# Kernel tuning notes

Measured on AMD Instinct MI355X. Metric: run time of the kernel, lower is better.

Reference implementation:

```python
import jax, jax.numpy as jnp
import numpy as np
from jax import lax

B, L, E = 2, 2048, 1024          # batch, seq_len, embed_dim
NL = 2                            # n_layers
DI = 2 * E                        # d_inner (expand=2)
DS = 16                           # d_state
DC = 4                            # d_conv
DTR = (E + 15) // 16              # dt_rank = ceil(d_model/16) = 64


def setup_inputs() -> dict:
    key = jax.random.key(0)
    ks = jax.random.split(key, 12)
    s = 0.02
    inp = {
        "x": jax.random.normal(ks[0], (B, L, E), jnp.float32),
        "pos_embed": jax.random.normal(ks[1], (L, E), jnp.float32) * s,
        "in_proj_w": jax.random.normal(ks[2], (NL, 2 * DI, E), jnp.float32) * s,
        "conv_w": jax.random.normal(ks[3], (NL, DI, DC), jnp.float32) * s,
        "conv_b": jnp.zeros((NL, DI), jnp.float32),
        "x_proj_w": jax.random.normal(ks[4], (NL, DTR + 2 * DS, DI), jnp.float32) * s,
        "dt_proj_w": jax.random.normal(ks[5], (NL, DI, DTR), jnp.float32) * s,
        "dt_bias": jax.random.normal(ks[6], (NL, DI), jnp.float32) * 0.1,
        "A_log": jnp.broadcast_to(jnp.log(jnp.arange(1, DS + 1, dtype=jnp.float32)), (NL, DI, DS)) + 0.0,
        "D_skip": jnp.ones((NL, DI), jnp.float32),
        "out_proj_w": jax.random.normal(ks[7], (NL, E, DI), jnp.float32) * s,
        "norm_w": jnp.ones((NL, E), jnp.float32),
    }
    return inp


def _rmsnorm(x, w, eps=1e-6):
    return x * lax.rsqrt(jnp.mean(x * x, axis=-1, keepdims=True) + eps) * w


def _mamba(h, in_w, cw, cb, xw, dtw, dtb, A_log, Dp, ow):
    # h: (B, L, E)
    xz = jnp.einsum("ble,de->bld", h, in_w)          # (B, L, 2*DI)
    xc, z = jnp.split(xz, 2, axis=-1)                 # each (B, L, DI)
    # causal depthwise conv1d (kernel DC)
    xp = jnp.pad(xc, ((0, 0), (DC - 1, 0), (0, 0)))
    xconv = cb
    acc = jnp.zeros_like(xc)
    for k in range(DC):
        acc = acc + cw[:, k] * xp[:, k:k + xc.shape[1], :]
    xc = jax.nn.silu(acc + cb)
    # input-dependent SSM params
    x_dbl = jnp.einsum("bld,rd->blr", xc, xw)         # (B, L, DTR+2*DS)
    dt, Bm, C = jnp.split(x_dbl, [DTR, DTR + DS], axis=-1)
    delta = jax.nn.softplus(jnp.einsum("blr,dr->bld", dt, dtw) + dtb)  # (B, L, DI)
    A = -jnp.exp(A_log)                               # (DI, DS)

    def step(hst, inp):
        d, bm, c, u = inp                             # (B,DI),(B,DS),(B,DS),(B,DI)
        hst = jnp.exp(d[..., None] * A) * hst + (d * u)[..., None] * bm[:, None, :]
        y = jnp.einsum("bdn,bn->bd", hst, c)
        return hst, y

    h0 = jnp.zeros((h.shape[0], DI, DS), h.dtype)
    _, ys = lax.scan(step, h0, (delta.swapaxes(0, 1), Bm.swapaxes(0, 1),
                                C.swapaxes(0, 1), xc.swapaxes(0, 1)))
    y = ys.swapaxes(0, 1) + xc * Dp                   # (B, L, DI)
    y = y * jax.nn.silu(z)
    return jnp.einsum("bld,ed->ble", y, ow)


def reference(x, pos_embed, in_proj_w, conv_w, conv_b, x_proj_w, dt_proj_w,
              dt_bias, A_log, D_skip, out_proj_w, norm_w):
    h = x + pos_embed[None, :x.shape[1]]
    for i in range(in_proj_w.shape[0]):
        y = _mamba(h, in_proj_w[i], conv_w[i], conv_b[i], x_proj_w[i],
                   dt_proj_w[i], dt_bias[i], A_log[i], D_skip[i], out_proj_w[i])
        h = _rmsnorm(y + h, norm_w[i])
    return h
```

## Files before the change

### kernel.cpp

```cpp
#include <hip/hip_runtime.h>

#define B_   2
#define L_   2048
#define E_   1024
#define NL_  2
#define DI_  2048
#define DS_  16
#define DC_  4
#define DTR_ 64
#define NXD_ 96
#define M_   (B_ * L_)
#define NCH_ 64
#define LC_  32

typedef __attribute__((ext_vector_type(8))) short bf16x8;
typedef __attribute__((ext_vector_type(4))) float f32x4;

__device__ __forceinline__ float bf2f(unsigned short u) {
    return __uint_as_float(((unsigned)u) << 16);
}
__device__ __forceinline__ unsigned short f2bf(float f) {
    unsigned u = __float_as_uint(f);
    u += 0x7fff + ((u >> 16) & 1);
    return (unsigned short)(u >> 16);
}

#define LOG2E_ 1.44269504f
#define LN2_   0.69314718f

__device__ __forceinline__ float sigmoidf_(float x) {
    return __builtin_amdgcn_rcpf(1.f + __builtin_amdgcn_exp2f(-x * LOG2E_));
}
__device__ __forceinline__ float softplusf_(float x) {
    float e = __builtin_amdgcn_exp2f(x * LOG2E_);
    float s = LN2_ * __builtin_amdgcn_logf(1.f + e);
    return x > 15.f ? x : s;
}
__device__ __forceinline__ float expf_(float x) {
    return __builtin_amdgcn_exp2f(x * LOG2E_);
}
__device__ __forceinline__ float ldin(const void* p, size_t i, int isbf) {
    return isbf ? bf2f(((const unsigned short*)p)[i]) : ((const float*)p)[i];
}
__device__ __forceinline__ void gld_lds16(const unsigned short* g, unsigned short* l) {
    __builtin_amdgcn_global_load_lds(
        (const __attribute__((address_space(1))) unsigned int*)g,
        (__attribute__((address_space(3))) unsigned int*)l, 16, 0, 0);
}
__device__ __forceinline__ bf16x8 ds_read128_(unsigned byteoff) {
    bf16x8 r;
    asm volatile("ds_read_b128 %0, %1" : "=&v"(r) : "v"(byteoff));
    return r;
}

__device__ __forceinline__ void expvec(int fast, float dv, const float* a2, float* e) {
    if (fast) {
        float p1 = __builtin_amdgcn_exp2f(dv * a2[0]);
        float p2 = p1 * p1, p4 = p2 * p2, p8 = p4 * p4;
        e[0] = p1;        e[1] = p2;        e[2] = p2 * p1;   e[3] = p4;
        e[4] = p4 * p1;   e[5] = p4 * p2;   e[6] = e[5] * p1; e[7] = p8;
        e[8] = p8 * p1;   e[9] = p8 * p2;   e[10] = e[9] * p1; e[11] = p8 * p4;
        e[12] = e[11] * p1; e[13] = e[11] * p2; e[14] = e[13] * p1; e[15] = p8 * p8;
    } else {
#pragma unroll
        for (int n = 0; n < 16; ++n) e[n] = __builtin_amdgcn_exp2f(dv * a2[n]);
    }
}

__global__ __launch_bounds__(256) void detect_kernel(const unsigned* __restrict__ x,
                                                     int* __restrict__ flags)
{
    __shared__ int cnt;
    if (threadIdx.x == 0) cnt = 0;
    __syncthreads();
    unsigned v = x[threadIdx.x];
    int e = (v >> 7) & 0xFF;
    if (e >= 90 && e <= 140) atomicAdd(&cnt, 1);
    __syncthreads();
    if (threadIdx.x == 0) {
        flags[0] = (cnt >= 192) ? 1 : 0;
        flags[1] = 1;
        flags[2] = 1;
    }
}

__global__ __launch_bounds__(256) void chk_alog(
    const void* __restrict__ alog, int* __restrict__ flags)
{
    int isbf = flags[0];
    int i = blockIdx.x * 256 + threadIdx.x;
    int layer = i / (DI_ * DS_);
    int n = i & (DS_ - 1);
    float a  = -expf_(ldin(alog, i, isbf));
    float a0 = -expf_(ldin(alog, i - n, isbf));
    float want = (n + 1) * a0;
    if (fabsf(a - want) > 0.02f * fabsf(want))
        atomicAnd(&flags[1 + layer], 0);
}

#define WB_IN_  0
#define WB_XW_  4194304
#define WB_DTW_ 4456448
#define WB_OW_  4587520
#define WB_TOT_ 6684672
__global__ __launch_bounds__(256) void cvt_layer_kernel(
    const void* __restrict__ inw, const void* __restrict__ xw,
    const void* __restrict__ dtw, const void* __restrict__ ow,
    int layer, unsigned short* __restrict__ wbuf, const int* __restrict__ flag,
    const void* __restrict__ cw, size_t cwoff, const void* __restrict__ cb,
    size_t cboff, float* __restrict__ cwT, float* __restrict__ cbF)
{
    int isbf = *flag;
    if (blockIdx.x < DI_ / 256) {
        int d = blockIdx.x * 256 + threadIdx.x;
#pragma unroll
        for (int k = 0; k < DC_; ++k)
            cwT[k * DI_ + d] = ldin(cw, cwoff + (size_t)d * DC_ + k, isbf);
        cbF[d] = ldin(cb, cboff + d, isbf);
    }
    int i = blockIdx.x * 256 + threadIdx.x;
    if (isbf && (i < WB_XW_ || i >= WB_DTW_)) return;
    unsigned short v;
    if (i < WB_XW_) {
        v = isbf ? ((const unsigned short*)inw)[(size_t)layer * 2 * DI_ * E_ + i]
                 : f2bf(((const float*)inw)[(size_t)layer * 2 * DI_ * E_ + i]);
    } else if (i < WB_DTW_) {
        int j = i - WB_XW_; int r = j >> 11, k = j & (DI_ - 1);
        v = (r < NXD_)
          ? (isbf ? ((const unsigned short*)xw)[(size_t)layer * NXD_ * DI_ + (size_t)r * DI_ + k]
                  : f2bf(((const float*)xw)[(size_t)layer * NXD_ * DI_ + (size_t)r * DI_ + k]))
          : (unsigned short)0;
    } else if (i < WB_OW_) {
        int j = i - WB_DTW_;
        v = isbf ? ((const unsigned short*)dtw)[(size_t)layer * DI_ * DTR_ + j]
                 : f2bf(((const float*)dtw)[(size_t)layer * DI_ * DTR_ + j]);
    } else {
        int j = i - WB_OW_;
        v = isbf ? ((const unsigned short*)ow)[(size_t)layer * E_ * DI_ + j]
                 : f2bf(((const float*)ow)[(size_t)layer * E_ * DI_ + j]);
    }
    wbuf[i] = v;
}

__global__ __launch_bounds__(256) void add_pos_kernel(
    const void* __restrict__ x, const void* __restrict__ pos,
    float* __restrict__ h, unsigned short* __restrict__ h16,
    const int* __restrict__ flag)
{
    int isbf = *flag;
    int i4 = (blockIdx.x * 256 + threadIdx.x) * 4;
#pragma unroll
    for (int q = 0; q < 4; ++q) {
        int i = i4 + q;
        float v = ldin(x, i, isbf) + ldin(pos, i & (L_ * E_ - 1), isbf);
        h[i] = v;
        h16[i] = f2bf(v);
    }
}

__global__ __launch_bounds__(256) void gemm_mfma(
    const unsigned short* __restrict__ A, int lda,
    const unsigned short* __restrict__ W, int ldw,
    void* __restrict__ C, int ldc, int Ksplit, size_t cSliceStride,
    const void* __restrict__ bias, size_t boff,
    void* __restrict__ C2, int ep, const int* __restrict__ flag,
    const unsigned short* __restrict__ Worig)
{
    __shared__ unsigned short As[128 * 64];
    __shared__ unsigned short Bs[128 * 64];
    int isbf = flag ? *flag : 1;
    const unsigned short* Wp = (Worig && isbf) ? Worig : W;
    int tid = threadIdx.x;
    int lane = tid & 63, w = tid >> 6;
    int m0 = blockIdx.x * 128, n0 = blockIdx.y * 128;
    int wm = (w >> 1) * 64, wn = (w & 1) * 64;
    int col = lane & 15, quad = lane >> 4;
    int kstart = blockIdx.z * Ksplit;

    f32x4 acc[4][4];
#pragma unroll
    for (int i = 0; i < 4; ++i)
#pragma unroll
        for (int j = 0; j < 4; ++j)
            acc[i][j] = (f32x4){0.f, 0.f, 0.f, 0.f};

    for (int kt = kstart; kt < kstart + Ksplit; kt += 64) {
#pragma unroll
        for (int i = 0; i < 4; ++i) {
            int seg = i * 4 + w;
            int q = seg * 64 + lane;
            int r = q >> 3, cd = q & 7;
            int cs = cd ^ (r & 7);
            gld_lds16(A + (size_t)(m0 + r) * lda + kt + cs * 8, &As[seg * 512]);
            gld_lds16(Wp + (size_t)(n0 + r) * ldw + kt + cs * 8, &Bs[seg * 512]);
        }
        __syncthreads();
#pragma unroll
        for (int ks = 0; ks < 2; ++ks) {
            bf16x8 af[4], bfr[4];
#pragma unroll
            for (int t = 0; t < 4; ++t) {
                int rowA = wm + t * 16 + col;
                int ca = ks * 4 + quad;
                af[t]  = *(const bf16x8*)&As[rowA * 64 + ((ca ^ (rowA & 7)) * 8)];
                int rowB = wn + t * 16 + col;
                bfr[t] = *(const bf16x8*)&Bs[rowB * 64 + ((ca ^ (rowB & 7)) * 8)];
            }
#pragma unroll
            for (int tm = 0; tm < 4; ++tm)
#pragma unroll
                for (int tn = 0; tn < 4; ++tn)
                    acc[tm][tn] = __builtin_amdgcn_mfma_f32_16x16x32_bf16(
                        af[tm], bfr[tn], acc[tm][tn], 0, 0, 0);
        }
        __syncthreads();
    }

    float* Cp = (float*)C + (size_t)blockIdx.z * cSliceStride;
#pragma unroll
    for (int tm = 0; tm < 4; ++tm)
#pragma unroll
        for (int tn = 0; tn < 4; ++tn)
#pragma unroll
            for (int rg = 0; rg < 4; ++rg) {
                int gm = m0 + wm + tm * 16 + quad * 4 + rg;
                int gn = n0 + wn + tn * 16 + col;
                float v = acc[tm][tn][rg];
                if (ep == 0) {
                    Cp[(size_t)gm * ldc + gn] = v;
                } else {
                    v = softplusf_(v + ldin(bias, boff + gn, isbf));
                    ((unsigned short*)C)[(size_t)gm * ldc + gn] = f2bf(v);
                }
            }
}

template <int KS, int MH, int RB, int CHK>
__device__ __forceinline__ void g8_phase(
    unsigned baseA, unsigned baseB,
    bf16x8 (&af)[4], bf16x8 (&bfr)[4], f32x4 (&acc)[8][4],
    int doStage, int st_t, int st_isB, int st_ks,
    const unsigned short* srcA, const unsigned short* srcW,
    unsigned short* ldsb, int w)
{
    if (RB) {
#pragma unroll
        for (int j = 0; j < 4; ++j)
            bfr[j] = ds_read128_(baseB + j * 2048 + KS * 1024);
    }
#pragma unroll
    for (int f = 0; f < 4; ++f)
        af[f] = ds_read128_(baseA + MH * 8192 + f * 2048 + KS * 1024);
    if (doStage) {
        const unsigned short* s0 = (st_isB ? srcW : srcA)
            + (size_t)w * 16 * E_ + st_t * 64 + st_ks * 32;
        unsigned short* d0 = ldsb + (st_t & 1) * 32768 + st_isB * 16384
            + w * 1024 + st_ks * 512;
        gld_lds16(s0, d0);
        gld_lds16(s0 + (size_t)8 * 16 * E_, d0 + 8 * 1024);
    }
    __builtin_amdgcn_s_barrier();
    asm volatile("s_waitcnt lgkmcnt(0)" ::: "memory");
    __builtin_amdgcn_sched_barrier(0);
    __builtin_amdgcn_s_setprio(1);
#pragma unroll
    for (int f = 0; f < 4; ++f)
#pragma unroll
        for (int j = 0; j < 4; ++j)
            acc[MH * 4 + f][j] = __builtin_amdgcn_mfma_f32_16x16x32_bf16(
                af[f], bfr[j], acc[MH * 4 + f][j], 0, 0, 0);
    __builtin_amdgcn_s_setprio(0);
    if (CHK == 8) { asm volatile("s_waitcnt vmcnt(8)" ::: "memory"); __builtin_amdgcn_sched_barrier(0); }
    if (CHK == 4) { asm volatile("s_waitcnt vmcnt(4)" ::: "memory"); __builtin_amdgcn_sched_barrier(0); }
    if (CHK == 0) { asm volatile("s_waitcnt vmcnt(0)"  ::: "memory"); __builtin_amdgcn_sched_barrier(0); }
    __builtin_amdgcn_s_barrier();
}

__global__ __launch_bounds__(512) void gemm_inproj8(
    const unsigned short* __restrict__ A,
    const unsigned short* __restrict__ Wbuf,
    const unsigned short* __restrict__ Worig,
    const int* __restrict__ flag,
    unsigned short* __restrict__ Cx,
    unsigned short* __restrict__ Cz)
{
    __shared__ unsigned short lds[65536];
    const unsigned short* W = (*flag) ? Worig : Wbuf;
    int tid = threadIdx.x;
    int lane = tid & 63, w = tid >> 6;
    int wr = w >> 2, wc = w & 3;
    int col = lane & 15, quad = lane >> 4;

    int flat = blockIdx.y * 16 + blockIdx.x;
    int nn = (flat & 7) * 32 + (flat >> 3);
    int cch = nn >> 5, wi = nn & 31;
    int bx = (cch & 3) * 4 + (wi & 3);
    int by = (cch >> 2) * 8 + (wi >> 2);
    int m0 = bx * 256, n0 = by * 256;

    const unsigned short* srcA = A + (size_t)(m0 + (lane & 15)) * E_ + (lane >> 4) * 8;
    const unsigned short* srcW = W + (size_t)(n0 + (lane & 15)) * E_ + (lane >> 4) * 8;

    unsigned baseA0 = (unsigned)(wr * 8 * 2048 + quad * 256 + col * 16);
    unsigned baseB0 = (unsigned)(32768 + wc * 4 * 2048 + quad * 256 + col * 16);
    unsigned baseA1 = baseA0 + 65536, baseB1 = baseB0 + 65536;

    f32x4 acc[8][4];
#pragma unroll
    for (int i = 0; i < 8; ++i)
#pragma unroll
        for (int j = 0; j < 4; ++j)
            acc[i][j] = (f32x4){0.f, 0.f, 0.f, 0.f};
    bf16x8 af[4], bfr[4];

#define G8STAGE(t_, isB_, ks_) { \
    const unsigned short* s0 = ((isB_) ? srcW : srcA) + (size_t)w * 16 * E_ + (t_) * 64 + (ks_) * 32; \
    unsigned short* d0 = lds + ((t_) & 1) * 32768 + (isB_) * 16384 + w * 1024 + (ks_) * 512; \
    gld_lds16(s0, d0); gld_lds16(s0 + (size_t)8 * 16 * E_, d0 + 8 * 1024); }

    G8STAGE(0, 0, 0) G8STAGE(0, 1, 0) G8STAGE(0, 0, 1) G8STAGE(0, 1, 1)
    G8STAGE(1, 0, 0) G8STAGE(1, 1, 0)
    asm volatile("s_waitcnt vmcnt(8)" ::: "memory");
    __builtin_amdgcn_sched_barrier(0);
    __builtin_amdgcn_s_barrier();

    for (int i = 0; i < 7; ++i) {
        int t1 = 2 * i + 1, t2 = 2 * i + 2, t3 = 2 * i + 3;
        g8_phase<0,0,1,-1>(baseA0, baseB0, af, bfr, acc, 1, t1, 0, 1, srcA, srcW, lds, w);
        g8_phase<0,1,0, 8>(baseA0, baseB0, af, bfr, acc, 1, t1, 1, 1, srcA, srcW, lds, w);
        g8_phase<1,0,1,-1>(baseA0, baseB0, af, bfr, acc, 1, t2, 0, 0, srcA, srcW, lds, w);
        g8_phase<1,1,0, 8>(baseA0, baseB0, af, bfr, acc, 1, t2, 1, 0, srcA, srcW, lds, w);
        g8_phase<0,0,1,-1>(baseA1, baseB1, af, bfr, acc, 1, t2, 0, 1, srcA, srcW, lds, w);
        g8_phase<0,1,0, 8>(baseA1, baseB1, af, bfr, acc, 1, t2, 1, 1, srcA, srcW, lds, w);
        g8_phase<1,0,1,-1>(baseA1, baseB1, af, bfr, acc, 1, t3, 0, 0, srcA, srcW, lds, w);
        g8_phase<1,1,0, 8>(baseA1, baseB1, af, bfr, acc, 1, t3, 1, 0, srcA, srcW, lds, w);
    }
    g8_phase<0,0,1,-1>(baseA0, baseB0, af, bfr, acc, 1, 15, 0, 1, srcA, srcW, lds, w);
    g8_phase<0,1,0, 8>(baseA0, baseB0, af, bfr, acc, 1, 15, 1, 1, srcA, srcW, lds, w);
    g8_phase<1,0,1,-1>(baseA0, baseB0, af, bfr, acc, 0, 0, 0, 0, srcA, srcW, lds, w);
    g8_phase<1,1,0, 4>(baseA0, baseB0, af, bfr, acc, 0, 0, 0, 0, srcA, srcW, lds, w);
    g8_phase<0,0,1,-1>(baseA1, baseB1, af, bfr, acc, 0, 0, 0, 0, srcA, srcW, lds, w);
    g8_phase<0,1,0, 0>(baseA1, baseB1, af, bfr, acc, 0, 0, 0, 0, srcA, srcW, lds, w);
    g8_phase<1,0,1,-1>(baseA1, baseB1, af, bfr, acc, 0, 0, 0, 0, srcA, srcW, lds, w);
    g8_phase<1,1,0,-1>(baseA1, baseB1, af, bfr, acc, 0, 0, 0, 0, srcA, srcW, lds, w);

    unsigned short* dst = (n0 < DI_) ? Cx : Cz;
    int nb = (n0 < DI_) ? n0 : n0 - DI_;
#pragma unroll
    for (int tm = 0; tm < 8; ++tm)
#pragma unroll
        for (int tn = 0; tn < 4; ++tn)
#pragma unroll
            for (int rg = 0; rg < 4; ++rg) {
                int gm = m0 + wr * 128 + tm * 16 + quad * 4 + rg;
                int gn = nb + wc * 64 + tn * 16 + col;
                dst[(size_t)gm * DI_ + gn] = f2bf(acc[tm][tn][rg]);
            }
#undef G8STAGE
}

__global__ __launch_bounds__(256) void xproj_reduce(
    const float* __restrict__ part, float* __restrict__ xdbl,
    unsigned short* __restrict__ dt16)
{
    int i = blockIdx.x * 256 + threadIdx.x;
    int r = i >> 7, c = i & 127;
    float v = 0.f;
#pragma unroll
    for (int s = 0; s < 8; ++s) v += part[(size_t)s * (M_ * 128) + i];
    if (c < NXD_) xdbl[(size_t)r * NXD_ + c] = v;
    if (c < DTR_) dt16[(size_t)r * DTR_ + c] = f2bf(v);
}

#define CT_ 4
__global__ __launch_bounds__(256) void conv_silu_v(
    const unsigned short* __restrict__ xcr16, const float* __restrict__ cwT,
    const float* __restrict__ cbF, unsigned short* __restrict__ xc16)
{
    int g = blockIdx.x;
    int bl0 = g * CT_;
    int l0 = bl0 & (L_ - 1);
    int d = threadIdx.x * 8;

    float w[DC_][8], bias[8];
#pragma unroll
    for (int k = 0; k < DC_; ++k) {
        *(float4*)&w[k][0] = *(const float4*)&cwT[k * DI_ + d];
        *(float4*)&w[k][4] = *(const float4*)&cwT[k * DI_ + d + 4];
    }
    *(float4*)&bias[0] = *(const float4*)&cbF[d];
    *(float4*)&bias[4] = *(const float4*)&cbF[d + 4];

    float xr[DC_ - 1 + CT_][8];
#pragma unroll
    for (int r = 0; r < DC_ - 1 + CT_; ++r) {
        int l = l0 - (DC_ - 1) + r;
        if (l >= 0) {
            bf16x8 v = *(const bf16x8*)&xcr16[(size_t)(bl0 - (DC_ - 1) + r) * DI_ + d];
#pragma unroll
            for (int j = 0; j < 8; ++j) xr[r][j] = bf2f((unsigned short)v[j]);
        } else {
#pragma unroll
            for (int j = 0; j < 8; ++j) xr[r][j] = 0.f;
        }
    }

#pragma unroll
    for (int t = 0; t < CT_; ++t) {
        float acc[8];
#pragma unroll
        for (int j = 0; j < 8; ++j) acc[j] = bias[j];
#pragma unroll
        for (int k = 0; k < DC_; ++k)
#pragma unroll
            for (int j = 0; j < 8; ++j)
                acc[j] = fmaf(w[k][j], xr[t + k][j], acc[j]);
        bf16x8 ov;
#pragma unroll
        for (int j = 0; j < 8; ++j) {
            float s = acc[j] * sigmoidf_(acc[j]);
            ov[j] = (short)f2bf(s);
        }
        *(bf16x8*)&xc16[(size_t)(bl0 + t) * DI_ + d] = ov;
    }
}

__global__ __launch_bounds__(256) void scan_part1(
    const unsigned short* __restrict__ dl16, const unsigned short* __restrict__ xc16,
    const float* __restrict__ xdbl,
    const void* __restrict__ A_log, size_t aoff,
    float* __restrict__ sumdbuf, float* __restrict__ scrS,
    const int* __restrict__ flags, int layer)
{
    int isbf = flags[0], fast = flags[1 + layer];
    __shared__ float bs[LC_][16];
    int c = blockIdx.y;
    int b = blockIdx.x >> 3;
    int d = ((blockIdx.x & 7) << 8) + threadIdx.x;
    for (int i = threadIdx.x; i < LC_ * 16; i += 256) {
        int l = i >> 4, n = i & 15;
        bs[l][n] = xdbl[((size_t)b * L_ + c * LC_ + l) * NXD_ + DTR_ + n];
    }
    __syncthreads();
    float a2[16];
#pragma unroll
    for (int n = 0; n < 16; ++n)
        a2[n] = -expf_(ldin(A_log, aoff + (size_t)d * DS_ + n, isbf)) * LOG2E_;
    float s[16] = {};
    float sumd = 0.f;
    const unsigned short* dp = dl16 + ((size_t)b * L_ + c * LC_) * DI_ + d;
    const unsigned short* up = xc16 + ((size_t)b * L_ + c * LC_) * DI_ + d;
    for (int l0 = 0; l0 < LC_; l0 += 4) {
        float dvv[4], uv[4];
#pragma unroll
        for (int q = 0; q < 4; ++q) {
            dvv[q] = bf2f(dp[(size_t)(l0 + q) * DI_]);
            uv[q]  = bf2f(up[(size_t)(l0 + q) * DI_]);
        }
#pragma unroll
        for (int q = 0; q < 4; ++q) {
            int l = l0 + q;
            float dv = dvv[q];
            sumd += dv;
            float dvu = dv * uv[q];
            float e[16];
            expvec(fast, dv, a2, e);
            float4 b0 = *(const float4*)&bs[l][0];
            float4 b1 = *(const float4*)&bs[l][4];
            float4 b2 = *(const float4*)&bs[l][8];
            float4 b3 = *(const float4*)&bs[l][12];
            float bv[16] = {b0.x,b0.y,b0.z,b0.w, b1.x,b1.y,b1.z,b1.w,
                            b2.x,b2.y,b2.z,b2.w, b3.x,b3.y,b3.z,b3.w};
#pragma unroll
            for (int n = 0; n < 16; ++n)
                s[n] = fmaf(e[n], s[n], dvu * bv[n]);
        }
    }
    int g = b * DI_ + d;
    sumdbuf[(size_t)c * (B_ * DI_) + g] = sumd;
    size_t base = ((size_t)c * (B_ * DI_) + g) * 16;
#pragma unroll
    for (int q = 0; q < 4; ++q)
        *(float4*)&scrS[base + q * 4] =
            make_float4(s[q*4], s[q*4+1], s[q*4+2], s[q*4+3]);
}

__global__ __launch_bounds__(256) void scan_combine(
    const float* __restrict__ sumdbuf, float* __restrict__ scrS,
    const void* __restrict__ A_log, size_t aoff, const int* __restrict__ flags)
{
    int isbf = flags[0];
    int t = blockIdx.x * 256 + threadIdx.x;
    int g = t >> 4, n = t & 15;
    int d = g & (DI_ - 1);
    float a2 = -expf_(ldin(A_log, aoff + (size_t)d * DS_ + n, isbf)) * LOG2E_;
    float sd[NCH_], sl[NCH_];
#pragma unroll
    for (int c = 0; c < NCH_; ++c) {
        sd[c] = sumdbuf[(size_t)c * (B_ * DI_) + g];
        sl[c] = scrS[(size_t)c * (B_ * DI_ * 16) + t];
    }
    float s = 0.f;
#pragma unroll
    for (int c = 0; c < NCH_; ++c) {
        float P = __builtin_amdgcn_exp2f(a2 * sd[c]);
        float nxt = fmaf(P, s, sl[c]);
        scrS[(size_t)c * (B_ * DI_ * 16) + t] = s;
        s = nxt;
    }
}

__global__ __launch_bounds__(256) void scan_part2(
    const unsigned short* __restrict__ dl16, unsigned short* __restrict__ xc16,
    const float* __restrict__ xdbl, const unsigned short* __restrict__ z,
    const void* __restrict__ A_log, size_t aoff,
    const void* __restrict__ Dskip, size_t doff,
    const float* __restrict__ scrS, const int* __restrict__ flags, int layer)
{
    int isbf = flags[0], fast = flags[1 + layer];
    __shared__ float bs[LC_][32];
    int c = blockIdx.y;
    int b = blockIdx.x >> 3;
    int d = ((blockIdx.x & 7) << 8) + threadIdx.x;
    for (int i = threadIdx.x; i < LC_ * 32; i += 256) {
        int l = i >> 5, n = i & 31;
        bs[l][n] = xdbl[((size_t)b * L_ + c * LC_ + l) * NXD_ + DTR_ + n];
    }
    __syncthreads();
    float a2[16];
#pragma unroll
    for (int n = 0; n < 16; ++n)
        a2[n] = -expf_(ldin(A_log, aoff + (size_t)d * DS_ + n, isbf)) * LOG2E_;
    float Dv = ldin(Dskip, doff + d, isbf);
    int g = b * DI_ + d;
    size_t sbase = ((size_t)c * (B_ * DI_) + g) * 16;
    float s[16];
#pragma unroll
    for (int q = 0; q < 4; ++q) {
        float4 sv = *(const float4*)&scrS[sbase + q * 4];
        s[q*4] = sv.x; s[q*4+1] = sv.y; s[q*4+2] = sv.z; s[q*4+3] = sv.w;
    }

    const unsigned short* dp = dl16 + ((size_t)b * L_ + c * LC_) * DI_ + d;
    unsigned short* up = xc16 + ((size_t)b * L_ + c * LC_) * DI_ + d;
    const unsigned short* zp = z + ((size_t)b * L_ + c * LC_) * DI_ + d;
    for (int l0 = 0; l0 < LC_; l0 += 4) {
        float dvv[4], uv[4], zv[4];
#pragma unroll
        for (int q = 0; q < 4; ++q) {
            dvv[q] = bf2f(dp[(size_t)(l0 + q) * DI_]);
            uv[q]  = bf2f(up[(size_t)(l0 + q) * DI_]);
            zv[q]  = bf2f(zp[(size_t)(l0 + q) * DI_]);
        }
#pragma unroll
        for (int q = 0; q < 4; ++q) {
            int l = l0 + q;
            float dv = dvv[q], u = uv[q];
            float dvu = dv * u;
            float e[16];
            expvec(fast, dv, a2, e);
            float4 b0 = *(const float4*)&bs[l][0];
            float4 b1 = *(const float4*)&bs[l][4];
            float4 b2 = *(const float4*)&bs[l][8];
            float4 b3 = *(const float4*)&bs[l][12];
            float4 c0 = *(const float4*)&bs[l][16];
            float4 c1 = *(const float4*)&bs[l][20];
            float4 c2 = *(const float4*)&bs[l][24];
            float4 c3 = *(const float4*)&bs[l][28];
            float bv[16] = {b0.x,b0.y,b0.z,b0.w, b1.x,b1.y,b1.z,b1.w,
                            b2.x,b2.y,b2.z,b2.w, b3.x,b3.y,b3.z,b3.w};
            float cv[16] = {c0.x,c0.y,c0.z,c0.w, c1.x,c1.y,c1.z,c1.w,
                            c2.x,c2.y,c2.z,c2.w, c3.x,c3.y,c3.z,c3.w};
            float y = 0.f;
#pragma unroll
            for (int n = 0; n < 16; ++n) {
                s[n] = fmaf(e[n], s[n], dvu * bv[n]);
                y = fmaf(s[n], cv[n], y);
            }
            float zvv = zv[q];
            up[(size_t)l * DI_] = f2bf((y + u * Dv) * (zvv * sigmoidf_(zvv)));
        }
    }
}

__global__ __launch_bounds__(256) void rmsnorm_kernel(
    const float* __restrict__ y0, const float* __restrict__ y1,
    float* __restrict__ h, unsigned short* __restrict__ h16,
    const void* __restrict__ nw, size_t nwoff, void* __restrict__ out,
    int write_out, const int* __restrict__ flag)
{
    int isbf = *flag;
    __shared__ float red[4];
    int row = blockIdx.x;
    float* hp = h + (size_t)row * E_;
    float v[4]; float ss = 0.f;
#pragma unroll
    for (int i = 0; i < 4; ++i) {
        int e = threadIdx.x + i * 256;
        size_t idx = (size_t)row * E_ + e;
        v[i] = y0[idx] + y1[idx] + hp[e];
        ss += v[i] * v[i];
    }
#pragma unroll
    for (int off = 1; off < 64; off <<= 1) ss += __shfl_xor(ss, off, 64);
    if ((threadIdx.x & 63) == 0) red[threadIdx.x >> 6] = ss;
    __syncthreads();
    ss = red[0] + red[1] + red[2] + red[3];
    float scale = rsqrtf(ss * (1.f / E_) + 1e-6f);
#pragma unroll
    for (int i = 0; i < 4; ++i) {
        int e = threadIdx.x + i * 256;
        float hv = v[i] * scale * ldin(nw, nwoff + e, isbf);
        hp[e] = hv;
        h16[(size_t)row * E_ + e] = f2bf(hv);
        if (write_out) {
            size_t oi = (size_t)row * E_ + e;
            if (isbf) ((unsigned short*)out)[oi] = f2bf(hv);
            else      ((float*)out)[oi] = hv;
        }
    }
}

extern "C" void kernel_launch(void* const* d_in, const int* in_sizes, int n_in,
                              void* d_out, int out_size, void* d_ws, size_t ws_size,
                              hipStream_t stream)
{
    const void* x    = d_in[0];
    const void* pos  = d_in[1];
    const void* inw  = d_in[2];
    const void* cw   = d_in[3];
    const void* cb   = d_in[4];
    const void* xw   = d_in[5];
    const void* dtw  = d_in[6];
    const void* dtb  = d_in[7];
    const void* alog = d_in[8];
    const void* dsk  = d_in[9];
    const void* ow   = d_in[10];
    const void* nw   = d_in[11];

    float* ws = (float*)d_ws;
    float* h      = ws;
    unsigned short* h16  = (unsigned short*)(ws + 4194304);
    unsigned short* z16  = (unsigned short*)(ws + 6291456);
    unsigned short* xc16 = (unsigned short*)(ws + 10485760);
    float* D      = ws + 14680064;
    float* R      = ws + 23068672;
    float* xdbl   = ws + 27262976;
    unsigned short* dt16 = (unsigned short*)(ws + 27656192);
    float* sumd   = ws + 27787264;
    unsigned short* wbuf = (unsigned short*)(ws + 28049408);
    int* flags    = (int*)(ws + 31391744);

    unsigned short* xcr16 = (unsigned short*)R;
    float* xp_part = R;
    float* scrS    = R;
    unsigned short* dl16 = (unsigned short*)D;
    float* yout0 = D;
    float* yout1 = D + (size_t)M_ * E_;
    float* cwT = sumd;
    float* cbF = sumd + DC_ * DI_;

    detect_kernel<<<1, 256, 0, stream>>>((const unsigned*)x, flags);
    chk_alog<<<NL_ * DI_ * DS_ / 256, 256, 0, stream>>>(alog, flags);
    add_pos_kernel<<<M_ * E_ / 1024, 256, 0, stream>>>(x, pos, h, h16, flags);

    for (int layer = 0; layer < NL_; ++layer) {
        const unsigned short* inws = (const unsigned short*)inw + (size_t)layer * 2 * DI_ * E_;
        const unsigned short* dtws = (const unsigned short*)dtw + (size_t)layer * DI_ * DTR_;
        const unsigned short* ows  = (const unsigned short*)ow  + (size_t)layer * E_ * DI_;

        cvt_layer_kernel<<<WB_TOT_ / 256, 256, 0, stream>>>(
            inw, xw, dtw, ow, layer, wbuf, flags,
            cw, (size_t)layer * DI_ * DC_, cb, (size_t)layer * DI_, cwT, cbF);

        gemm_inproj8<<<dim3(M_ / 256, 2 * DI_ / 256, 1), 512, 0, stream>>>(
            h16, wbuf + WB_IN_, inws, flags, xcr16, z16);
        conv_silu_v<<<M_ / CT_, 256, 0, stream>>>(xcr16, cwT, cbF, xc16);
        gemm_mfma<<<dim3(M_ / 128, 1, 8), 256, 0, stream>>>(
            xc16, DI_, wbuf + WB_XW_, DI_, xp_part, 128, DI_ / 8, (size_t)M_ * 128,
            nullptr, 0, nullptr, 0, flags, nullptr);
        xproj_reduce<<<M_ * 128 / 256, 256, 0, stream>>>(xp_part, xdbl, dt16);
        gemm_mfma<<<dim3(M_ / 128, DI_ / 128, 1), 256, 0, stream>>>(
            dt16, DTR_, wbuf + WB_DTW_, DTR_, dl16, DI_, DTR_, 0,
            dtb, (size_t)layer * DI_, nullptr, 2, flags, dtws);
        scan_part1<<<dim3(B_ * DI_ / 256, NCH_), 256, 0, stream>>>(
            dl16, xc16, xdbl, alog, (size_t)layer * DI_ * DS_, sumd, scrS, flags, layer);
        scan_combine<<<B_ * DI_ * DS_ / 256, 256, 0, stream>>>(
            sumd, scrS, alog, (size_t)layer * DI_ * DS_, flags);
        scan_part2<<<dim3(B_ * DI_ / 256, NCH_), 256, 0, stream>>>(
            dl16, xc16, xdbl, z16, alog, (size_t)layer * DI_ * DS_,
            dsk, (size_t)layer * DI_, scrS, flags, layer);
        gemm_mfma<<<dim3(M_ / 128, E_ / 128, 2), 256, 0, stream>>>(
            xc16, DI_, wbuf + WB_OW_, DI_, yout0, E_, DI_ / 2, (size_t)M_ * E_,
            nullptr, 0, nullptr, 0, flags, ows);
        rmsnorm_kernel<<<M_, 256, 0, stream>>>(
            yout0, yout1, h, h16, nw, (size_t)layer * E_, d_out,
            layer == NL_ - 1 ? 1 : 0, flags);
    }
}
```

Baseline: 558.0 us.

## Fuse chunked scan phases into one cooperative kernel with grid syncs

Replaces the three scan kernels (per-chunk partial scan, cross-chunk combine, final scan with output gating) with one cooperative kernel that separates the phases with grid-wide syncs. The B and C vectors are staged into shared memory once and reused by both scan passes. This is meant to remove two kernel launches and their gaps, plus the repeated shared-memory staging. In exchange, all 1024 blocks must be co-resident, which forces a min-blocks launch bound that can raise register pressure. If the cooperative launch fails, the code falls back to the original three kernels.

```diff
diff --git a/kernel.cpp b/kernel.cpp
--- a/kernel.cpp
+++ b/kernel.cpp
@@ -1,4 +1,6 @@
 #include <hip/hip_runtime.h>
+#include <hip/hip_cooperative_groups.h>
+namespace cg = cooperative_groups;
 
 #define B_   2
 #define L_   2048
@@ -425,6 +427,153 @@
     }
 }
 
+__global__ __launch_bounds__(256, 4) void scan_fused(
+    const unsigned short* __restrict__ dl16, unsigned short* __restrict__ xc16,
+    const float* __restrict__ xdbl, const unsigned short* __restrict__ z,
+    const void* __restrict__ A_log, size_t aoff,
+    const void* __restrict__ Dskip, size_t doff,
+    float* __restrict__ sumdbuf, float* __restrict__ scrS,
+    const int* __restrict__ flags, int layer)
+{
+    int isbf = flags[0], fast = flags[1 + layer];
+    __shared__ float bs[LC_][32];
+    int c = blockIdx.y;
+    int b = blockIdx.x >> 3;
+    int d = ((blockIdx.x & 7) << 8) + threadIdx.x;
+    for (int i = threadIdx.x; i < LC_ * 32; i += 256) {
+        int l = i >> 5, n = i & 31;
+        bs[l][n] = xdbl[((size_t)b * L_ + c * LC_ + l) * NXD_ + DTR_ + n];
+    }
+    __syncthreads();
+    float a2[16];
+#pragma unroll
+    for (int n = 0; n < 16; ++n)
+        a2[n] = -expf_(ldin(A_log, aoff + (size_t)d * DS_ + n, isbf)) * LOG2E_;
+    int g = b * DI_ + d;
+    const unsigned short* dp = dl16 + ((size_t)b * L_ + c * LC_) * DI_ + d;
+    unsigned short* up = xc16 + ((size_t)b * L_ + c * LC_) * DI_ + d;
+
+    {
+        float s[16] = {};
+        float sumd = 0.f;
+        for (int l0 = 0; l0 < LC_; l0 += 4) {
+            float dvv[4], uv[4];
+#pragma unroll
+            for (int q = 0; q < 4; ++q) {
+                dvv[q] = bf2f(dp[(size_t)(l0 + q) * DI_]);
+                uv[q]  = bf2f(up[(size_t)(l0 + q) * DI_]);
+            }
+#pragma unroll
+            for (int q = 0; q < 4; ++q) {
+                int l = l0 + q;
+                float dv = dvv[q];
+                sumd += dv;
+                float dvu = dv * uv[q];
+                float e[16];
+                expvec(fast, dv, a2, e);
+                float4 b0 = *(const float4*)&bs[l][0];
+                float4 b1 = *(const float4*)&bs[l][4];
+                float4 b2 = *(const float4*)&bs[l][8];
+                float4 b3 = *(const float4*)&bs[l][12];
+                float bv[16] = {b0.x,b0.y,b0.z,b0.w, b1.x,b1.y,b1.z,b1.w,
+                                b2.x,b2.y,b2.z,b2.w, b3.x,b3.y,b3.z,b3.w};
+#pragma unroll
+                for (int n = 0; n < 16; ++n)
+                    s[n] = fmaf(e[n], s[n], dvu * bv[n]);
+            }
+        }
+        sumdbuf[(size_t)c * (B_ * DI_) + g] = sumd;
+        size_t base = ((size_t)c * (B_ * DI_) + g) * 16;
+#pragma unroll
+        for (int q = 0; q < 4; ++q)
+            *(float4*)&scrS[base + q * 4] =
+                make_float4(s[q*4], s[q*4+1], s[q*4+2], s[q*4+3]);
+    }
+
+    __threadfence();
+    cg::this_grid().sync();
+
+    {
+        int flat = (blockIdx.y * 16 + blockIdx.x) * 256 + threadIdx.x;
+        if (flat < B_ * DI_ * DS_) {
+            int t = flat;
+            int gg = t >> 4, n = t & 15;
+            int dd = gg & (DI_ - 1);
+            float a2c = -expf_(ldin(A_log, aoff + (size_t)dd * DS_ + n, isbf)) * LOG2E_;
+            float s = 0.f;
+            for (int cb = 0; cb < NCH_ / 16; ++cb) {
+                float sd[16], sl[16];
+#pragma unroll
+                for (int j = 0; j < 16; ++j) {
+                    int cc = cb * 16 + j;
+                    sd[j] = sumdbuf[(size_t)cc * (B_ * DI_) + gg];
+                    sl[j] = scrS[(size_t)cc * (B_ * DI_ * 16) + t];
+                }
+#pragma unroll
+                for (int j = 0; j < 16; ++j) {
+                    int cc = cb * 16 + j;
+                    float P = __builtin_amdgcn_exp2f(a2c * sd[j]);
+                    float nxt = fmaf(P, s, sl[j]);
+                    scrS[(size_t)cc * (B_ * DI_ * 16) + t] = s;
+                    s = nxt;
+                }
+            }
+        }
+    }
+
+    __threadfence();
+    cg::this_grid().sync();
+
+    {
+        float Dv = ldin(Dskip, doff + d, isbf);
+        size_t sbase = ((size_t)c * (B_ * DI_) + g) * 16;
+        float s[16];
+#pragma unroll
+        for (int q = 0; q < 4; ++q) {
+            float4 sv = *(const float4*)&scrS[sbase + q * 4];
+            s[q*4] = sv.x; s[q*4+1] = sv.y; s[q*4+2] = sv.z; s[q*4+3] = sv.w;
+        }
+        const unsigned short* zp = z + ((size_t)b * L_ + c * LC_) * DI_ + d;
+        for (int l0 = 0; l0 < LC_; l0 += 4) {
+            float dvv[4], uv[4], zv[4];
+#pragma unroll
+            for (int q = 0; q < 4; ++q) {
+                dvv[q] = bf2f(dp[(size_t)(l0 + q) * DI_]);
+                uv[q]  = bf2f(up[(size_t)(l0 + q) * DI_]);
+                zv[q]  = bf2f(zp[(size_t)(l0 + q) * DI_]);
+            }
+#pragma unroll
+            for (int q = 0; q < 4; ++q) {
+                int l = l0 + q;
+                float dv = dvv[q], u = uv[q];
+                float dvu = dv * u;
+                float e[16];
+                expvec(fast, dv, a2, e);
+                float4 b0 = *(const float4*)&bs[l][0];
+                float4 b1 = *(const float4*)&bs[l][4];
+                float4 b2 = *(const float4*)&bs[l][8];
+                float4 b3 = *(const float4*)&bs[l][12];
+                float4 c0 = *(const float4*)&bs[l][16];
+                float4 c1 = *(const float4*)&bs[l][20];
+                float4 c2 = *(const float4*)&bs[l][24];
+                float4 c3 = *(const float4*)&bs[l][28];
+                float bv[16] = {b0.x,b0.y,b0.z,b0.w, b1.x,b1.y,b1.z,b1.w,
+                                b2.x,b2.y,b2.z,b2.w, b3.x,b3.y,b3.z,b3.w};
+                float cv[16] = {c0.x,c0.y,c0.z,c0.w, c1.x,c1.y,c1.z,c1.w,
+                                c2.x,c2.y,c2.z,c2.w, c3.x,c3.y,c3.z,c3.w};
+                float y = 0.f;
+#pragma unroll
+                for (int n = 0; n < 16; ++n) {
+                    s[n] = fmaf(e[n], s[n], dvu * bv[n]);
+                    y = fmaf(s[n], cv[n], y);
+                }
+                float zvv = zv[q];
+                up[(size_t)l * DI_] = f2bf((y + u * Dv) * (zvv * sigmoidf_(zvv)));
+            }
+        }
+    }
+}
+
 __global__ __launch_bounds__(256) void scan_part1(
     const unsigned short* __restrict__ dl16, const unsigned short* __restrict__ xc16,
     const float* __restrict__ xdbl,
@@ -683,13 +832,37 @@
         gemm_mfma<<<dim3(M_ / 128, DI_ / 128, 1), 256, 0, stream>>>(
             dt16, DTR_, wbuf + WB_DTW_, DTR_, dl16, DI_, DTR_, 0,
             dtb, (size_t)layer * DI_, nullptr, 2, flags, dtws);
-        scan_part1<<<dim3(B_ * DI_ / 256, NCH_), 256, 0, stream>>>(
-            dl16, xc16, xdbl, alog, (size_t)layer * DI_ * DS_, sumd, scrS, flags, layer);
-        scan_combine<<<B_ * DI_ * DS_ / 256, 256, 0, stream>>>(
-            sumd, scrS, alog, (size_t)layer * DI_ * DS_, flags);
-        scan_part2<<<dim3(B_ * DI_ / 256, NCH_), 256, 0, stream>>>(
-            dl16, xc16, xdbl, z16, alog, (size_t)layer * DI_ * DS_,
-            dsk, (size_t)layer * DI_, scrS, flags, layer);
+
+        {
+            size_t aoff = (size_t)layer * DI_ * DS_;
+            size_t doff = (size_t)layer * DI_;
+            const unsigned short* dl16a = dl16;
+            unsigned short* xc16a = xc16;
+            const float* xdbla = xdbl;
+            const unsigned short* z16a = z16;
+            const void* aloga = alog;
+            const void* dska = dsk;
+            float* sumda = sumd;
+            float* scrSa = scrS;
+            const int* flagsa = flags;
+            int layera = layer;
+            void* args[] = { (void*)&dl16a, (void*)&xc16a, (void*)&xdbla,
+                             (void*)&z16a, (void*)&aloga, (void*)&aoff,
+                             (void*)&dska, (void*)&doff, (void*)&sumda,
+                             (void*)&scrSa, (void*)&flagsa, (void*)&layera };
+            hipError_t err = hipLaunchCooperativeKernel(
+                (const void*)scan_fused, dim3(B_ * DI_ / 256, NCH_), dim3(256),
+                args, 0, stream);
+            if (err != hipSuccess) {
+                scan_part1<<<dim3(B_ * DI_ / 256, NCH_), 256, 0, stream>>>(
+                    dl16, xc16, xdbl, alog, aoff, sumd, scrS, flags, layer);
+                scan_combine<<<B_ * DI_ * DS_ / 256, 256, 0, stream>>>(
+                    sumd, scrS, alog, aoff, flags);
+                scan_part2<<<dim3(B_ * DI_ / 256, NCH_), 256, 0, stream>>>(
+                    dl16, xc16, xdbl, z16, alog, aoff, dsk, doff, scrS, flags, layer);
+            }
+        }
+
         gemm_mfma<<<dim3(M_ / 128, E_ / 128, 2), 256, 0, stream>>>(
             xc16, DI_, wbuf + WB_OW_, DI_, yout0, E_, DI_ / 2, (size_t)M_ * E_,
             nullptr, 0, nullptr, 0, flags, ows);
```

Result: slower. 1.505 ms (+169.7%).
